# Kernel tuning notes

Hardware: AMD Instinct MI355X
Metric: run time of the kernel (lower is better)

Reference implementation:

```python
import jax, jax.numpy as jnp
import numpy as np

# config matching init_kwargs
B, LQ, LKV = 2, 1024, 1024
H, DQK, DV = 8, 64, 64
DQ = DK = DVIN = DOUT = 512
SPAN, STRIDE = 128, 1


def setup_inputs() -> dict:
    key = jax.random.key(0)
    ks = jax.random.split(key, 7)
    q = jax.random.normal(ks[0], (B, LQ, DQ), jnp.float32)
    k = jax.random.normal(ks[1], (B, LKV, DK), jnp.float32)
    v = jax.random.normal(ks[2], (B, LKV, DVIN), jnp.float32)
    # nn.Linear(bias=False) weights, stored as [in, out] for x @ W
    Wq = jax.random.normal(ks[3], (DQ, H * DQK), jnp.float32) / np.sqrt(DQ).astype(np.float32)
    Wk = jax.random.normal(ks[4], (DK, H * DQK), jnp.float32) / np.sqrt(DK).astype(np.float32)
    Wv = jax.random.normal(ks[5], (DVIN, H * DV), jnp.float32) / np.sqrt(DVIN).astype(np.float32)
    Wo = jax.random.normal(ks[6], (H * DV, DOUT), jnp.float32) / np.sqrt(H * DV).astype(np.float32)
    return dict(q=q, k=k, v=v, Wq=Wq, Wk=Wk, Wv=Wv, Wo=Wo)


def reference(q, k, v, Wq, Wk, Wv, Wo):
    b = q.shape[0]
    Q = (q @ Wq).reshape(b, LQ, H, DQK).transpose(0, 2, 1, 3)    # [b,H,LQ,DQK]
    K = (k @ Wk).reshape(b, LKV, H, DQK).transpose(0, 2, 1, 3)   # [b,H,LKV,DQK]
    V = (v @ Wv).reshape(b, LKV, H, DV).transpose(0, 2, 1, 3)    # [b,H,LKV,DV]

    # banded window indices: kvi[i, j] = i - (span-1) + stride*j
    row = jnp.arange(SPAN)[:, None]
    col = jnp.arange(LQ)[None, :]
    kvi = row - (SPAN - 1) + STRIDE * col                         # [SPAN, LQ]
    valid = (kvi >= 0) & (kvi < LKV)
    kvi_c = jnp.clip(kvi, 0, LKV - 1)

    Kw = K[:, :, kvi_c, :]                                        # [b,H,SPAN,LQ,DQK]
    scores = jnp.einsum('bhjd,bhsjd->bhsj', Q, Kw) / np.float32(np.sqrt(DQK))
    scores = jnp.where(valid[None, None], scores, -jnp.inf)
    w = jax.nn.softmax(scores, axis=2)                            # softmax over span (dim=2)

    Vw = V[:, :, kvi_c, :]                                        # [b,H,SPAN,LQ,DV]
    out_h = jnp.einsum('bhsj,bhsjd->bhjd', w, Vw)                 # [b,H,LQ,DV]
    out = out_h.transpose(0, 2, 1, 3).reshape(b, LQ, H * DV)
    return out @ Wo
```

## Files before the change

kernel.cpp:

```cpp
#include <hip/hip_runtime.h>
#include <hip/hip_bf16.h>

#define LQ 1024
#define NH 8
#define DHEAD 64
#define DMODEL 512
#define SPAN 128
#define MROWS 2048

typedef __attribute__((ext_vector_type(8))) short   bf16x8;
typedef __attribute__((ext_vector_type(4))) float   f32x4;
typedef __attribute__((ext_vector_type(8))) unsigned short us8;

static __device__ __forceinline__ unsigned short f2bf(float f) {
    union { __hip_bfloat16 h; unsigned short u; } cv;
    cv.h = __float2bfloat16(f);
    return cv.u;
}

static __device__ __forceinline__ void gload_lds16(const void* g, void* l) {
    __builtin_amdgcn_global_load_lds((const __attribute__((address_space(1))) void*)g,
                                     (__attribute__((address_space(3))) void*)l, 16, 0, 0);
}

__global__ __launch_bounds__(256) void transposeW(
    const float* __restrict__ W0, const float* __restrict__ W1,
    const float* __restrict__ W2, const float* __restrict__ W3,
    unsigned short* __restrict__ T0, unsigned short* __restrict__ T1,
    unsigned short* __restrict__ T2, unsigned short* __restrict__ T3)
{
    const float* W = blockIdx.z == 0 ? W0 : blockIdx.z == 1 ? W1 : blockIdx.z == 2 ? W2 : W3;
    unsigned short* T = blockIdx.z == 0 ? T0 : blockIdx.z == 1 ? T1 : blockIdx.z == 2 ? T2 : T3;
    __shared__ unsigned short sT[64][72];
    int c = threadIdx.x & 63;
    int r0 = (threadIdx.x >> 6) * 16;
    int n0 = blockIdx.x * 64, k0 = blockIdx.y * 64;
    #pragma unroll
    for (int i = 0; i < 16; ++i) {
        int r = r0 + i;
        sT[c][r] = f2bf(W[(size_t)(k0 + r) * DMODEL + n0 + c]);
    }
    __syncthreads();
    #pragma unroll
    for (int i = 0; i < 16; ++i) {
        int r = r0 + i;
        T[(size_t)(n0 + r) * DMODEL + k0 + c] = sT[r][c];
    }
}

__global__ __launch_bounds__(256) void gemm_qkv(
    const float* __restrict__ q, const float* __restrict__ k, const float* __restrict__ v,
    const unsigned short* __restrict__ WtQ, const unsigned short* __restrict__ WtK,
    const unsigned short* __restrict__ WtV,
    unsigned short* __restrict__ Qp, unsigned short* __restrict__ Kp,
    unsigned short* __restrict__ Vt)
{
    __shared__ unsigned short As[2][4096];
    __shared__ unsigned short Bs[2][4096];

    const int z = blockIdx.z;
    const float* A = z == 0 ? q : (z == 1 ? k : v);
    const unsigned short* Bt = z == 0 ? WtQ : (z == 1 ? WtK : WtV);
    unsigned short* C = z == 0 ? Qp : (z == 1 ? Kp : Vt);
    const bool mode2 = (z == 2);

    const int tid = threadIdx.x;
    const int lane = tid & 63;
    const int w = tid >> 6;
    const int wm = w >> 1, wn = w & 1;
    const int m0 = blockIdx.y * 64;
    const int n0 = blockIdx.x * 64;

    const int srow = lane >> 3;
    const int sgrp = (lane & 7) ^ srow;

    f32x4 acc[2][2];
    #pragma unroll
    for (int i = 0; i < 2; ++i)
        #pragma unroll
        for (int j = 0; j < 2; ++j)
            acc[i][j] = f32x4{0.f, 0.f, 0.f, 0.f};

    auto stageB = [&](int buf, int kt) {
        const int k0 = kt * 64;
        #pragma unroll
        for (int cc = 0; cc < 2; ++cc) {
            int call = w * 2 + cc;
            int row = call * 8 + srow;
            gload_lds16(Bt + (size_t)(n0 + row) * DMODEL + k0 + (sgrp << 3),
                        &Bs[buf][call * 512]);
        }
    };

    float4 areg[2][2];
    auto loadA = [&](int kt) {
        const int k0 = kt * 64;
        #pragma unroll
        for (int i = 0; i < 2; ++i) {
            int c = i * 256 + tid;
            int row = c >> 3, g = c & 7;
            const float* p = A + (size_t)(m0 + row) * DMODEL + k0 + g * 8;
            areg[i][0] = *(const float4*)p;
            areg[i][1] = *(const float4*)(p + 4);
        }
    };
    auto writeA = [&](int buf) {
        #pragma unroll
        for (int i = 0; i < 2; ++i) {
            int c = i * 256 + tid;
            int row = c >> 3, g = c & 7;
            us8 t;
            t[0] = f2bf(areg[i][0].x); t[1] = f2bf(areg[i][0].y);
            t[2] = f2bf(areg[i][0].z); t[3] = f2bf(areg[i][0].w);
            t[4] = f2bf(areg[i][1].x); t[5] = f2bf(areg[i][1].y);
            t[6] = f2bf(areg[i][1].z); t[7] = f2bf(areg[i][1].w);
            *(us8*)&As[buf][row * 64 + ((g ^ (row & 7)) << 3)] = t;
        }
    };

    const int frow = lane & 15;
    const int fkg  = lane >> 4;

    auto ldfrag = [&](const unsigned short* base, int rb, int ks) -> bf16x8 {
        int row = rb * 16 + frow;
        int kg = ks * 4 + fkg;
        int off = row * 64 + ((kg ^ (row & 7)) << 3);
        return *(const bf16x8*)&base[off];
    };

    const unsigned short* aB[2] = { mode2 ? Bs[0] : As[0], mode2 ? Bs[1] : As[1] };
    const unsigned short* bB[2] = { mode2 ? As[0] : Bs[0], mode2 ? As[1] : Bs[1] };
    const int ra = mode2 ? wn : wm;
    const int rb_ = mode2 ? wm : wn;

    loadA(0);
    stageB(0, 0);
    writeA(0);
    __syncthreads();

    for (int kt = 0; kt < 8; ++kt) {
        int buf = kt & 1;
        if (kt < 7) { loadA(kt + 1); stageB(buf ^ 1, kt + 1); }
        #pragma unroll
        for (int ks = 0; ks < 2; ++ks) {
            bf16x8 a0 = ldfrag(aB[buf], ra * 2 + 0, ks);
            bf16x8 a1 = ldfrag(aB[buf], ra * 2 + 1, ks);
            bf16x8 b0 = ldfrag(bB[buf], rb_ * 2 + 0, ks);
            bf16x8 b1 = ldfrag(bB[buf], rb_ * 2 + 1, ks);
            acc[0][0] = __builtin_amdgcn_mfma_f32_16x16x32_bf16(a0, b0, acc[0][0], 0, 0, 0);
            acc[0][1] = __builtin_amdgcn_mfma_f32_16x16x32_bf16(a0, b1, acc[0][1], 0, 0, 0);
            acc[1][0] = __builtin_amdgcn_mfma_f32_16x16x32_bf16(a1, b0, acc[1][0], 0, 0, 0);
            acc[1][1] = __builtin_amdgcn_mfma_f32_16x16x32_bf16(a1, b1, acc[1][1], 0, 0, 0);
        }
        if (kt < 7) writeA(buf ^ 1);
        __syncthreads();
    }

    #pragma unroll
    for (int i = 0; i < 2; ++i) {
        #pragma unroll
        for (int j = 0; j < 2; ++j) {
            #pragma unroll
            for (int r = 0; r < 4; ++r) {
                if (mode2) {
                    int n = n0 + wn * 32 + i * 16 + (lane >> 4) * 4 + r;
                    int m = m0 + wm * 32 + j * 16 + (lane & 15);
                    int b = m >> 10, jq = m & 1023, h = n >> 6, d = n & 63;
                    C[(((size_t)(b * NH + h) * DHEAD) + d) * LQ + jq] = f2bf(acc[i][j][r]);
                } else {
                    int m = m0 + wm * 32 + i * 16 + (lane >> 4) * 4 + r;
                    int n = n0 + wn * 32 + j * 16 + (lane & 15);
                    int b = m >> 10, jq = m & 1023, h = n >> 6, d = n & 63;
                    C[(((size_t)(b * NH + h) * LQ) + jq) * DHEAD + d] = f2bf(acc[i][j][r]);
                }
            }
        }
    }
}

__global__ __launch_bounds__(256) void gemm_out(
    const unsigned short* __restrict__ A, const unsigned short* __restrict__ Bt,
    float* __restrict__ C)
{
    __shared__ unsigned short As[2][2048];
    __shared__ unsigned short Bs[2][4096];

    const int tid = threadIdx.x;
    const int lane = tid & 63;
    const int w = tid >> 6;
    const int m0 = blockIdx.y * 32;
    const int n0 = blockIdx.x * 64;

    const int srow = lane >> 3;
    const int sgrp = (lane & 7) ^ srow;

    f32x4 acc[2];
    acc[0] = f32x4{0.f, 0.f, 0.f, 0.f};
    acc[1] = f32x4{0.f, 0.f, 0.f, 0.f};

    auto stage = [&](int buf, int kt) {
        const int k0 = kt * 64;
        gload_lds16(A + (size_t)(m0 + w * 8 + srow) * DMODEL + k0 + (sgrp << 3),
                    &As[buf][w * 512]);
        #pragma unroll
        for (int cc = 0; cc < 2; ++cc) {
            int call = w * 2 + cc;
            int row = call * 8 + srow;
            gload_lds16(Bt + (size_t)(n0 + row) * DMODEL + k0 + (sgrp << 3),
                        &Bs[buf][call * 512]);
        }
    };

    const int frow = lane & 15;
    const int fkg  = lane >> 4;

    auto ldfrag = [&](const unsigned short* base, int rb, int ks) -> bf16x8 {
        int row = rb * 16 + frow;
        int kg = ks * 4 + fkg;
        int off = row * 64 + ((kg ^ (row & 7)) << 3);
        return *(const bf16x8*)&base[off];
    };

    stage(0, 0);
    __syncthreads();

    for (int kt = 0; kt < 8; ++kt) {
        int buf = kt & 1;
        if (kt < 7) stage(buf ^ 1, kt + 1);
        #pragma unroll
        for (int ks = 0; ks < 2; ++ks) {
            bf16x8 a0 = ldfrag(As[buf], 0, ks);
            bf16x8 a1 = ldfrag(As[buf], 1, ks);
            bf16x8 b0 = ldfrag(Bs[buf], w, ks);
            acc[0] = __builtin_amdgcn_mfma_f32_16x16x32_bf16(a0, b0, acc[0], 0, 0, 0);
            acc[1] = __builtin_amdgcn_mfma_f32_16x16x32_bf16(a1, b0, acc[1], 0, 0, 0);
        }
        __syncthreads();
    }

    #pragma unroll
    for (int i = 0; i < 2; ++i) {
        #pragma unroll
        for (int r = 0; r < 4; ++r) {
            int m = m0 + i * 16 + (lane >> 4) * 4 + r;
            int n = n0 + w * 16 + (lane & 15);
            C[(size_t)m * DMODEL + n] = acc[i][r];
        }
    }
}

__global__ __launch_bounds__(256) void attn_mfma(
    const unsigned short* __restrict__ Qp, const unsigned short* __restrict__ Kp,
    const unsigned short* __restrict__ Vt, unsigned short* __restrict__ O)
{
    __shared__ __align__(16) unsigned short Ks[192 * 64];
    __shared__ __align__(16) unsigned short Vs[64 * 192];
    __shared__ __align__(16) unsigned short Ps[64 * 200];

    const int tid = threadIdx.x;
    const int lane = tid & 63;
    const int w = tid >> 6;
    const int bh = blockIdx.y;
    const int j0 = blockIdx.x * 64;
    const int kv0 = j0 - 128;

    const unsigned short* Kg = Kp + (size_t)bh * LQ * DHEAD;
    const unsigned short* Vg = Vt + (size_t)bh * DHEAD * LQ;

    const us8 zz = {0, 0, 0, 0, 0, 0, 0, 0};

    us8 kreg[6];
    #pragma unroll
    for (int i = 0; i < 6; ++i) {
        int c = i * 256 + tid;
        int row = c >> 3, g = c & 7;
        int grow = kv0 + row;
        us8 t = zz;
        if (grow >= 0) t = *(const us8*)&Kg[(size_t)grow * DHEAD + g * 8];
        kreg[i] = t;
    }
    us8 vreg[6];
    #pragma unroll
    for (int i = 0; i < 6; ++i) {
        int c = i * 256 + tid;
        int d = c / 24, g = c - d * 24;
        int col = kv0 + g * 8;
        us8 t = zz;
        if (col >= 0) t = *(const us8*)&Vg[(size_t)d * LQ + col];
        vreg[i] = t;
    }
    #pragma unroll
    for (int i = 0; i < 6; ++i) {
        int c = i * 256 + tid;
        int row = c >> 3, g = c & 7;
        *(us8*)&Ks[row * 64 + ((g ^ (row & 7)) << 3)] = kreg[i];
    }
    #pragma unroll
    for (int i = 0; i < 6; ++i) {
        int c = i * 256 + tid;
        int d = c / 24, g = c - d * 24;
        int sg = (g & ~7) | ((g & 7) ^ (d & 7));
        *(us8*)&Vs[d * 192 + sg * 8] = vreg[i];
    }

    const int frow = lane & 15, fkg = lane >> 4;

    bf16x8 qa[2];
    {
        const unsigned short* Qrow = Qp + ((size_t)bh * LQ + j0 + w * 16 + frow) * DHEAD;
        qa[0] = *(const bf16x8*)&Qrow[fkg * 8];
        qa[1] = *(const bf16x8*)&Qrow[32 + fkg * 8];
    }

    __syncthreads();

    f32x4 sacc[12];
    #pragma unroll
    for (int b = 0; b < 12; ++b) sacc[b] = f32x4{0.f, 0.f, 0.f, 0.f};
    #pragma unroll
    for (int b = 0; b < 12; ++b) {
        #pragma unroll
        for (int ks = 0; ks < 2; ++ks) {
            int row = b * 16 + frow;
            int kg = ks * 4 + fkg;
            bf16x8 kb = *(const bf16x8*)&Ks[row * 64 + ((kg ^ (row & 7)) << 3)];
            sacc[b] = __builtin_amdgcn_mfma_f32_16x16x32_bf16(qa[ks], kb, sacc[b], 0, 0, 0);
        }
    }

    #pragma unroll
    for (int r = 0; r < 4; ++r) {
        int q = w * 16 + fkg * 4 + r;
        float sv[12];
        float mx = -1e30f;
        #pragma unroll
        for (int b = 0; b < 12; ++b) {
            int rel = b * 16 + frow - 128 - q;
            int kvabs = kv0 + b * 16 + frow;
            bool valid = (rel <= 0) & (rel >= -(SPAN - 1)) & (kvabs >= 0);
            float s = valid ? sacc[b][r] * 0.125f : -1e30f;
            sv[b] = s;
            mx = fmaxf(mx, s);
        }
        #pragma unroll
        for (int off = 1; off < 16; off <<= 1) mx = fmaxf(mx, __shfl_xor(mx, off));
        float sum = 0.f;
        #pragma unroll
        for (int b = 0; b < 12; ++b) { float p = __expf(sv[b] - mx); sv[b] = p; sum += p; }
        #pragma unroll
        for (int off = 1; off < 16; off <<= 1) sum += __shfl_xor(sum, off);
        float inv = 1.0f / sum;
        #pragma unroll
        for (int b = 0; b < 12; ++b) sacc[b][r] = sv[b] * inv;
    }

    #pragma unroll
    for (int b = 0; b < 12; ++b) {
        #pragma unroll
        for (int r = 0; r < 4; ++r) {
            int q = w * 16 + fkg * 4 + r;
            Ps[q * 200 + b * 16 + frow] = f2bf(sacc[b][r]);
        }
    }

    f32x4 oacc[4];
    #pragma unroll
    for (int nb = 0; nb < 4; ++nb) oacc[nb] = f32x4{0.f, 0.f, 0.f, 0.f};
    #pragma unroll
    for (int kb = 0; kb < 6; ++kb) {
        int q = w * 16 + frow;
        bf16x8 pa = *(const bf16x8*)&Ps[q * 200 + (kb * 4 + fkg) * 8];
        #pragma unroll
        for (int nb = 0; nb < 4; ++nb) {
            int d = nb * 16 + frow;
            int g = kb * 4 + fkg;
            int sg = (g & ~7) | ((g & 7) ^ (d & 7));
            bf16x8 vb = *(const bf16x8*)&Vs[d * 192 + sg * 8];
            oacc[nb] = __builtin_amdgcn_mfma_f32_16x16x32_bf16(pa, vb, oacc[nb], 0, 0, 0);
        }
    }

    int b = bh >> 3, h = bh & 7;
    #pragma unroll
    for (int nb = 0; nb < 4; ++nb) {
        #pragma unroll
        for (int r = 0; r < 4; ++r) {
            int jq = j0 + w * 16 + fkg * 4 + r;
            int col = h * 64 + nb * 16 + frow;
            O[(size_t)(b * LQ + jq) * DMODEL + col] = f2bf(oacc[nb][r]);
        }
    }
}

extern "C" void kernel_launch(void* const* d_in, const int* in_sizes, int n_in,
                              void* d_out, int out_size, void* d_ws, size_t ws_size,
                              hipStream_t stream) {
    const float* q  = (const float*)d_in[0];
    const float* k  = (const float*)d_in[1];
    const float* v  = (const float*)d_in[2];
    const float* Wq = (const float*)d_in[3];
    const float* Wk = (const float*)d_in[4];
    const float* Wv = (const float*)d_in[5];
    const float* Wo = (const float*)d_in[6];

    const size_t MK = (size_t)MROWS * DMODEL;
    const size_t WK = (size_t)DMODEL * DMODEL;

    unsigned short* WtQ = (unsigned short*)d_ws;
    unsigned short* WtK = WtQ + WK;
    unsigned short* WtV = WtK + WK;
    unsigned short* WtO = WtV + WK;
    unsigned short* Qp  = WtO + WK;
    unsigned short* Kp  = Qp + MK;
    unsigned short* Vt  = Kp + MK;
    unsigned short* Ah  = Vt + MK;

    transposeW<<<dim3(8, 8, 4), 256, 0, stream>>>(Wq, Wk, Wv, Wo, WtQ, WtK, WtV, WtO);

    gemm_qkv<<<dim3(8, 32, 3), 256, 0, stream>>>(q, k, v, WtQ, WtK, WtV, Qp, Kp, Vt);

    attn_mfma<<<dim3(LQ / 64, 16), 256, 0, stream>>>(Qp, Kp, Vt, Ah);

    gemm_out<<<dim3(8, 64), 256, 0, stream>>>(Ah, WtO, (float*)d_out);
}
```

Measured before the change: 42.26 us.

## Split K dimension across two wave groups in QKV and output GEMMs

Measured after the change: 41.48 us. Within noise of the previous version (-1.8%).

```diff
diff --git a/kernel.cpp b/kernel.cpp
--- a/kernel.cpp
+++ b/kernel.cpp
@@ -48,15 +48,15 @@
     }
 }
 
-__global__ __launch_bounds__(256) void gemm_qkv(
+__global__ __launch_bounds__(512, 4) void gemm_qkv(
     const float* __restrict__ q, const float* __restrict__ k, const float* __restrict__ v,
     const unsigned short* __restrict__ WtQ, const unsigned short* __restrict__ WtK,
     const unsigned short* __restrict__ WtV,
     unsigned short* __restrict__ Qp, unsigned short* __restrict__ Kp,
     unsigned short* __restrict__ Vt)
 {
-    __shared__ unsigned short As[2][4096];
-    __shared__ unsigned short Bs[2][4096];
+    __shared__ __align__(16) unsigned short As[2][2][4096];
+    __shared__ __align__(16) unsigned short Bs[2][2][4096];
 
     const int z = blockIdx.z;
     const float* A = z == 0 ? q : (z == 1 ? k : v);
@@ -67,7 +67,10 @@
     const int tid = threadIdx.x;
     const int lane = tid & 63;
     const int w = tid >> 6;
-    const int wm = w >> 1, wn = w & 1;
+    const int wg = w & 3;
+    const int half = w >> 2;
+    const int tidh = tid & 255;
+    const int wm = wg >> 1, wn = wg & 1;
     const int m0 = blockIdx.y * 64;
     const int n0 = blockIdx.x * 64;
 
@@ -81,23 +84,23 @@
         for (int j = 0; j < 2; ++j)
             acc[i][j] = f32x4{0.f, 0.f, 0.f, 0.f};
 
-    auto stageB = [&](int buf, int kt) {
-        const int k0 = kt * 64;
+    auto stageB = [&](int buf, int ktg) {
+        const int k0 = ktg * 64;
         #pragma unroll
         for (int cc = 0; cc < 2; ++cc) {
-            int call = w * 2 + cc;
+            int call = wg * 2 + cc;
             int row = call * 8 + srow;
             gload_lds16(Bt + (size_t)(n0 + row) * DMODEL + k0 + (sgrp << 3),
-                        &Bs[buf][call * 512]);
+                        &Bs[half][buf][call * 512]);
         }
     };
 
     float4 areg[2][2];
-    auto loadA = [&](int kt) {
-        const int k0 = kt * 64;
+    auto loadA = [&](int ktg) {
+        const int k0 = ktg * 64;
         #pragma unroll
         for (int i = 0; i < 2; ++i) {
-            int c = i * 256 + tid;
+            int c = i * 256 + tidh;
             int row = c >> 3, g = c & 7;
             const float* p = A + (size_t)(m0 + row) * DMODEL + k0 + g * 8;
             areg[i][0] = *(const float4*)p;
@@ -107,14 +110,14 @@
     auto writeA = [&](int buf) {
         #pragma unroll
         for (int i = 0; i < 2; ++i) {
-            int c = i * 256 + tid;
+            int c = i * 256 + tidh;
             int row = c >> 3, g = c & 7;
             us8 t;
             t[0] = f2bf(areg[i][0].x); t[1] = f2bf(areg[i][0].y);
             t[2] = f2bf(areg[i][0].z); t[3] = f2bf(areg[i][0].w);
             t[4] = f2bf(areg[i][1].x); t[5] = f2bf(areg[i][1].y);
             t[6] = f2bf(areg[i][1].z); t[7] = f2bf(areg[i][1].w);
-            *(us8*)&As[buf][row * 64 + ((g ^ (row & 7)) << 3)] = t;
+            *(us8*)&As[half][buf][row * 64 + ((g ^ (row & 7)) << 3)] = t;
         }
     };
 
@@ -128,19 +131,22 @@
         return *(const bf16x8*)&base[off];
     };
 
-    const unsigned short* aB[2] = { mode2 ? Bs[0] : As[0], mode2 ? Bs[1] : As[1] };
-    const unsigned short* bB[2] = { mode2 ? As[0] : Bs[0], mode2 ? As[1] : Bs[1] };
+    const unsigned short* aB[2] = { mode2 ? Bs[half][0] : As[half][0],
+                                    mode2 ? Bs[half][1] : As[half][1] };
+    const unsigned short* bB[2] = { mode2 ? As[half][0] : Bs[half][0],
+                                    mode2 ? As[half][1] : Bs[half][1] };
     const int ra = mode2 ? wn : wm;
     const int rb_ = mode2 ? wm : wn;
 
-    loadA(0);
-    stageB(0, 0);
+    const int ktbase = half * 4;
+    loadA(ktbase);
+    stageB(0, ktbase);
     writeA(0);
     __syncthreads();
 
-    for (int kt = 0; kt < 8; ++kt) {
-        int buf = kt & 1;
-        if (kt < 7) { loadA(kt + 1); stageB(buf ^ 1, kt + 1); }
+    for (int t = 0; t < 4; ++t) {
+        int buf = t & 1;
+        if (t < 3) { loadA(ktbase + t + 1); stageB(buf ^ 1, ktbase + t + 1); }
         #pragma unroll
         for (int ks = 0; ks < 2; ++ks) {
             bf16x8 a0 = ldfrag(aB[buf], ra * 2 + 0, ks);
@@ -152,42 +158,67 @@
             acc[1][0] = __builtin_amdgcn_mfma_f32_16x16x32_bf16(a1, b0, acc[1][0], 0, 0, 0);
             acc[1][1] = __builtin_amdgcn_mfma_f32_16x16x32_bf16(a1, b1, acc[1][1], 0, 0, 0);
         }
-        if (kt < 7) writeA(buf ^ 1);
+        if (t < 3) writeA(buf ^ 1);
         __syncthreads();
     }
 
-    #pragma unroll
-    for (int i = 0; i < 2; ++i) {
-        #pragma unroll
-        for (int j = 0; j < 2; ++j) {
+    float* red = (float*)&As[0][0][0];
+    if (half == 1) {
+        int base = (wg * 64 + lane) * 17;
+        #pragma unroll
+        for (int i = 0; i < 2; ++i)
             #pragma unroll
-            for (int r = 0; r < 4; ++r) {
-                if (mode2) {
-                    int n = n0 + wn * 32 + i * 16 + (lane >> 4) * 4 + r;
-                    int m = m0 + wm * 32 + j * 16 + (lane & 15);
-                    int b = m >> 10, jq = m & 1023, h = n >> 6, d = n & 63;
-                    C[(((size_t)(b * NH + h) * DHEAD) + d) * LQ + jq] = f2bf(acc[i][j][r]);
-                } else {
-                    int m = m0 + wm * 32 + i * 16 + (lane >> 4) * 4 + r;
-                    int n = n0 + wn * 32 + j * 16 + (lane & 15);
-                    int b = m >> 10, jq = m & 1023, h = n >> 6, d = n & 63;
-                    C[(((size_t)(b * NH + h) * LQ) + jq) * DHEAD + d] = f2bf(acc[i][j][r]);
+            for (int j = 0; j < 2; ++j)
+                #pragma unroll
+                for (int r = 0; r < 4; ++r)
+                    red[base + (i * 2 + j) * 4 + r] = acc[i][j][r];
+    }
+    __syncthreads();
+    if (half == 0) {
+        int base = (wg * 64 + lane) * 17;
+        #pragma unroll
+        for (int i = 0; i < 2; ++i)
+            #pragma unroll
+            for (int j = 0; j < 2; ++j)
+                #pragma unroll
+                for (int r = 0; r < 4; ++r)
+                    acc[i][j][r] += red[base + (i * 2 + j) * 4 + r];
+
+        #pragma unroll
+        for (int i = 0; i < 2; ++i) {
+            #pragma unroll
+            for (int j = 0; j < 2; ++j) {
+                #pragma unroll
+                for (int r = 0; r < 4; ++r) {
+                    if (mode2) {
+                        int n = n0 + wn * 32 + i * 16 + (lane >> 4) * 4 + r;
+                        int m = m0 + wm * 32 + j * 16 + (lane & 15);
+                        int b = m >> 10, jq = m & 1023, h = n >> 6, d = n & 63;
+                        C[(((size_t)(b * NH + h) * DHEAD) + d) * LQ + jq] = f2bf(acc[i][j][r]);
+                    } else {
+                        int m = m0 + wm * 32 + i * 16 + (lane >> 4) * 4 + r;
+                        int n = n0 + wn * 32 + j * 16 + (lane & 15);
+                        int b = m >> 10, jq = m & 1023, h = n >> 6, d = n & 63;
+                        C[(((size_t)(b * NH + h) * LQ) + jq) * DHEAD + d] = f2bf(acc[i][j][r]);
+                    }
                 }
             }
         }
     }
 }
 
-__global__ __launch_bounds__(256) void gemm_out(
+__global__ __launch_bounds__(512, 4) void gemm_out(
     const unsigned short* __restrict__ A, const unsigned short* __restrict__ Bt,
     float* __restrict__ C)
 {
-    __shared__ unsigned short As[2][2048];
-    __shared__ unsigned short Bs[2][4096];
+    __shared__ __align__(16) unsigned short As[2][2][2048];
+    __shared__ __align__(16) unsigned short Bs[2][2][4096];
 
     const int tid = threadIdx.x;
     const int lane = tid & 63;
     const int w = tid >> 6;
+    const int wg = w & 3;
+    const int half = w >> 2;
     const int m0 = blockIdx.y * 32;
     const int n0 = blockIdx.x * 64;
 
@@ -198,16 +229,16 @@
     acc[0] = f32x4{0.f, 0.f, 0.f, 0.f};
     acc[1] = f32x4{0.f, 0.f, 0.f, 0.f};
 
-    auto stage = [&](int buf, int kt) {
-        const int k0 = kt * 64;
-        gload_lds16(A + (size_t)(m0 + w * 8 + srow) * DMODEL + k0 + (sgrp << 3),
-                    &As[buf][w * 512]);
+    auto stage = [&](int buf, int ktg) {
+        const int k0 = ktg * 64;
+        gload_lds16(A + (size_t)(m0 + wg * 8 + srow) * DMODEL + k0 + (sgrp << 3),
+                    &As[half][buf][wg * 512]);
         #pragma unroll
         for (int cc = 0; cc < 2; ++cc) {
-            int call = w * 2 + cc;
+            int call = wg * 2 + cc;
             int row = call * 8 + srow;
             gload_lds16(Bt + (size_t)(n0 + row) * DMODEL + k0 + (sgrp << 3),
-                        &Bs[buf][call * 512]);
+                        &Bs[half][buf][call * 512]);
         }
     };
 
@@ -221,30 +252,45 @@
         return *(const bf16x8*)&base[off];
     };
 
-    stage(0, 0);
-    __syncthreads();
-
-    for (int kt = 0; kt < 8; ++kt) {
-        int buf = kt & 1;
-        if (kt < 7) stage(buf ^ 1, kt + 1);
+    const int ktbase = half * 4;
+    stage(0, ktbase);
+    __syncthreads();
+
+    for (int t = 0; t < 4; ++t) {
+        int buf = t & 1;
+        if (t < 3) stage(buf ^ 1, ktbase + t + 1);
         #pragma unroll
         for (int ks = 0; ks < 2; ++ks) {
-            bf16x8 a0 = ldfrag(As[buf], 0, ks);
-            bf16x8 a1 = ldfrag(As[buf], 1, ks);
-            bf16x8 b0 = ldfrag(Bs[buf], w, ks);
+            bf16x8 a0 = ldfrag(As[half][buf], 0, ks);
+            bf16x8 a1 = ldfrag(As[half][buf], 1, ks);
+            bf16x8 b0 = ldfrag(Bs[half][buf], wg, ks);
             acc[0] = __builtin_amdgcn_mfma_f32_16x16x32_bf16(a0, b0, acc[0], 0, 0, 0);
             acc[1] = __builtin_amdgcn_mfma_f32_16x16x32_bf16(a1, b0, acc[1], 0, 0, 0);
         }
         __syncthreads();
     }
 
-    #pragma unroll
-    for (int i = 0; i < 2; ++i) {
-        #pragma unroll
-        for (int r = 0; r < 4; ++r) {
-            int m = m0 + i * 16 + (lane >> 4) * 4 + r;
-            int n = n0 + w * 16 + (lane & 15);
-            C[(size_t)m * DMODEL + n] = acc[i][r];
+    float* red = (float*)&As[0][0][0];
+    if (half == 1) {
+        int base = (wg * 64 + lane) * 9;
+        #pragma unroll
+        for (int i = 0; i < 2; ++i)
+            #pragma unroll
+            for (int r = 0; r < 4; ++r)
+                red[base + i * 4 + r] = acc[i][r];
+    }
+    __syncthreads();
+    if (half == 0) {
+        int base = (wg * 64 + lane) * 9;
+        #pragma unroll
+        for (int i = 0; i < 2; ++i) {
+            #pragma unroll
+            for (int r = 0; r < 4; ++r) {
+                float vsum = acc[i][r] + red[base + i * 4 + r];
+                int m = m0 + i * 16 + (lane >> 4) * 4 + r;
+                int n = n0 + wg * 16 + (lane & 15);
+                C[(size_t)m * DMODEL + n] = vsum;
+            }
         }
     }
 }
@@ -417,9 +463,9 @@
 
     transposeW<<<dim3(8, 8, 4), 256, 0, stream>>>(Wq, Wk, Wv, Wo, WtQ, WtK, WtV, WtO);
 
-    gemm_qkv<<<dim3(8, 32, 3), 256, 0, stream>>>(q, k, v, WtQ, WtK, WtV, Qp, Kp, Vt);
+    gemm_qkv<<<dim3(8, 32, 3), 512, 0, stream>>>(q, k, v, WtQ, WtK, WtV, Qp, Kp, Vt);
 
     attn_mfma<<<dim3(LQ / 64, 16), 256, 0, stream>>>(Qp, Kp, Vt, Ah);
 
-    gemm_out<<<dim3(8, 64), 256, 0, stream>>>(Ah, WtO, (float*)d_out);
-}
+    gemm_out<<<dim3(8, 64), 512, 0, stream>>>(Ah, WtO, (float*)d_out);
+}
```
